# Optimization experiments

Hardware: AMD Instinct MI355X
Metric: run time of the kernel (lower is better)

The kernel has to match this reference:

```python
import jax, jax.numpy as jnp
import numpy as np

NCLASSES = 4
FG_THRESH = 0.5
MEANS = jnp.array([0.0, 0.0, 0.0, 0.0], dtype=jnp.float32)
STDS = jnp.array([0.1, 0.1, 0.2, 0.2], dtype=jnp.float32)
BBOX_INSIDE_W = jnp.array([1.0, 1.0, 1.0, 1.0], dtype=jnp.float32)


def _bbox_overlaps(boxes, gt):
    # boxes: (B,M,4), gt: (B,K,4) -> IoU (B,M,K), faithful to bbox_overlaps_batch
    aw = boxes[..., 2] - boxes[..., 0] + 1.0
    ah = boxes[..., 3] - boxes[..., 1] + 1.0
    gw = gt[..., 2] - gt[..., 0] + 1.0
    gh = gt[..., 3] - gt[..., 1] + 1.0
    area_a = aw * ah                      # (B,M)
    area_g = gw * gh                      # (B,K)
    ix1 = jnp.maximum(boxes[:, :, None, 0], gt[:, None, :, 0])
    iy1 = jnp.maximum(boxes[:, :, None, 1], gt[:, None, :, 1])
    ix2 = jnp.minimum(boxes[:, :, None, 2], gt[:, None, :, 2])
    iy2 = jnp.minimum(boxes[:, :, None, 3], gt[:, None, :, 3])
    iw = jnp.clip(ix2 - ix1 + 1.0, 0.0)
    ih = jnp.clip(iy2 - iy1 + 1.0, 0.0)
    inter = iw * ih                       # (B,M,K)
    ov = inter / (area_a[:, :, None] + area_g[:, None, :] - inter)
    gt_zero = (gw == 1.0) & (gh == 1.0)   # zero-area (padding) gt boxes
    an_zero = (aw == 1.0) & (ah == 1.0)
    ov = jnp.where(gt_zero[:, None, :], 0.0, ov)
    ov = jnp.where(an_zero[:, :, None], -1.0, ov)
    return ov


def _bbox_transform(ex, gt):
    ew = ex[..., 2] - ex[..., 0] + 1.0
    eh = ex[..., 3] - ex[..., 1] + 1.0
    ecx = ex[..., 0] + 0.5 * ew
    ecy = ex[..., 1] + 0.5 * eh
    gw = gt[..., 2] - gt[..., 0] + 1.0
    gh = gt[..., 3] - gt[..., 1] + 1.0
    gcx = gt[..., 0] + 0.5 * gw
    gcy = gt[..., 1] + 0.5 * gh
    dx = (gcx - ecx) / ew
    dy = (gcy - ecy) / eh
    dw = jnp.log(gw / ew)
    dh = jnp.log(gh / eh)
    return jnp.stack([dx, dy, dw, dh], axis=-1)


def setup_inputs() -> dict:
    key = jax.random.key(0)
    B, N, K = 16, 8192, 128
    ks = jax.random.split(key, 9)
    # valid proposal boxes inside an ~1242x375 (KITTI-like) image
    x1 = jax.random.uniform(ks[0], (B, N)) * 1000.0
    y1 = jax.random.uniform(ks[1], (B, N)) * 300.0
    bw = jax.random.uniform(ks[2], (B, N)) * 200.0 + 4.0
    bh = jax.random.uniform(ks[3], (B, N)) * 150.0 + 4.0
    all_rois = jnp.concatenate(
        [jnp.zeros((B, N, 1), jnp.float32),
         jnp.stack([x1, y1, x1 + bw, y1 + bh], axis=-1)], axis=-1)
    gx1 = jax.random.uniform(ks[4], (B, K)) * 1000.0
    gy1 = jax.random.uniform(ks[5], (B, K)) * 300.0
    gw = jax.random.uniform(ks[6], (B, K)) * 200.0 + 8.0
    gh = jax.random.uniform(ks[7], (B, K)) * 150.0 + 8.0
    cls = jax.random.randint(ks[8], (B, K), 1, NCLASSES).astype(jnp.float32)
    gt_boxes = jnp.stack([gx1, gy1, gx1 + gw, gy1 + gh, cls], axis=-1)
    return {"all_rois": all_rois, "gt_boxes": gt_boxes}


def reference(all_rois, gt_boxes):
    B = all_rois.shape[0]
    dt = all_rois.dtype
    # append gt boxes as extra rois: (0, x1, y1, x2, y2)
    gt_append = jnp.concatenate(
        [jnp.zeros_like(gt_boxes[..., :1]), gt_boxes[..., :4]], axis=-1)
    rois = jnp.concatenate([all_rois, gt_append], axis=1)   # (B,M,5)
    M = rois.shape[1]

    ov = _bbox_overlaps(rois[..., 1:5], gt_boxes[..., :4])  # (B,M,K)
    max_ov = ov.max(axis=2)                                 # (B,M)
    gt_assign = jnp.argmax(ov, axis=2)                      # (B,M)
    labels_all = jnp.take_along_axis(gt_boxes[..., 4], gt_assign, axis=1)

    # focal-loss path: fg = ov >= thresh, keep order = [fg asc, bg asc]
    fg = max_ov >= FG_THRESH
    order = jnp.argsort(jnp.where(fg, 0, 1).astype(jnp.int32), axis=1, stable=True)
    fg_count = fg.sum(axis=1)                               # (B,)
    pos = jnp.arange(M)[None, :]

    labels_perm = jnp.take_along_axis(labels_all, order, axis=1)
    labels_batch = jnp.where(pos < fg_count[:, None], labels_perm, 0.0)

    rois_perm = jnp.take_along_axis(rois, order[..., None], axis=1)
    rois_batch = rois_perm.at[..., 0].set(
        jnp.broadcast_to(jnp.arange(B, dtype=dt)[:, None], (B, M)))

    ga_perm = jnp.take_along_axis(gt_assign, order, axis=1)
    gt_rois = jnp.take_along_axis(gt_boxes, ga_perm[..., None], axis=1)  # (B,M,5)

    targets = _bbox_transform(rois_batch[..., 1:5], gt_rois[..., :4])
    targets = (targets - MEANS) / STDS
    bbox_targets = jnp.where((labels_batch > 0)[..., None], targets, 0.0)

    # focal inside weights in ORIGINAL roi order (as in the source), bg zeroed
    focal_w = jnp.where(fg, (1.0 - max_ov) ** 2, 0.0)       # (B,M)
    bbox_inside_weights = jnp.broadcast_to(focal_w[..., None], (B, M, 4))
    bbox_outside_weights = (bbox_inside_weights > 0).astype(dt)

    return (rois_batch, labels_batch, bbox_targets,
            bbox_inside_weights, bbox_outside_weights)
```

## Files before the change

kernel.cpp:

```cpp
#include <hip/hip_runtime.h>
#include <math.h>

#define BB 16
#define NN 8192
#define KK 128
#define MM (NN + KK)
#define NCHUNK 32


__global__ __launch_bounds__(256) void ptl_iou(
    const float* __restrict__ all_rois,
    const float* __restrict__ gt_boxes,
    int* __restrict__ chunk_counts,
    float2* __restrict__ pack,
    float* __restrict__ out_inside,
    float* __restrict__ out_outside)
{
    __shared__ float4 s_box[KK];
    __shared__ int    s_w[4];

    const int b    = blockIdx.y;
    const int cx   = blockIdx.x;
    const int tid  = threadIdx.x;
    const int lane = tid & 63, wv = tid >> 6;

    if (tid < KK) {
        const float* g = gt_boxes + ((size_t)b * KK + tid) * 5;
        float gx1 = g[0], gy1 = g[1], gx2 = g[2], gy2 = g[3];
        float gw = gx2 - gx1 + 1.0f, gh = gy2 - gy1 + 1.0f;
        bool z = (gw == 1.0f) && (gh == 1.0f);
        s_box[tid] = z ? make_float4(1e30f, 1e30f, -1e30f, -1e30f)
                       : make_float4(gx1, gy1, gx2 + 1.0f, gy2 + 1.0f);
    }
    __syncthreads();

    const int i = cx * 256 + tid;
    const float* rp_in = all_rois + ((size_t)b * NN + i) * 5;
    const float x1 = rp_in[1], y1 = rp_in[2], x2 = rp_in[3], y2 = rp_in[4];
    const float X2p = x2 + 1.0f, Y2p = y2 + 1.0f;
    const float aw = X2p - x1, ah = Y2p - y1;
    const float area_a = aw * ah;

    float best = -1e30f;
    int besti = 0;
    #pragma unroll 4
    for (int k = 0; k < KK; ++k) {
        float4 g = s_box[k];
        float area_g = (g.z - g.x) * (g.w - g.y);
        float iw = fmaxf(fminf(X2p, g.z) - fmaxf(x1, g.x), 0.0f);
        float ih = fmaxf(fminf(Y2p, g.w) - fmaxf(y1, g.y), 0.0f);
        float inter = iw * ih;
        float ov = inter / (area_a + area_g - inter);
        if (ov > best) { best = ov; besti = k; }
    }
    if (aw == 1.0f && ah == 1.0f) { best = -1.0f; besti = 0; }

    const bool fg = (best >= 0.5f);

    {
        const size_t idx = (size_t)b * MM + i;
        const float om = 1.0f - best;
        const float w  = fg ? om * om : 0.0f;
        const float ow = (w > 0.0f) ? 1.0f : 0.0f;
        ((float4*)out_inside)[idx]  = make_float4(w, w, w, w);
        ((float4*)out_outside)[idx] = make_float4(ow, ow, ow, ow);
    }
    if (cx == 0 && tid < KK) {
        const size_t idx = (size_t)b * MM + NN + tid;
        ((float4*)out_inside)[idx]  = make_float4(0.f, 0.f, 0.f, 0.f);
        ((float4*)out_outside)[idx] = make_float4(0.f, 0.f, 0.f, 0.f);
    }

    pack[(size_t)b * NN + i] = make_float2(best, __int_as_float(besti));

    unsigned long long m = __ballot(fg ? 1 : 0);
    if (lane == 0) s_w[wv] = __popcll(m);
    __syncthreads();
    if (tid == 0)
        chunk_counts[b * NCHUNK + cx] = s_w[0] + s_w[1] + s_w[2] + s_w[3];
}

__global__ __launch_bounds__(256) void ptl_scatter(
    const float* __restrict__ all_rois,
    const float* __restrict__ gt_boxes,
    const int* __restrict__ chunk_counts,
    const float2* __restrict__ pack,
    float* __restrict__ out_rois,
    float* __restrict__ out_labels,
    float* __restrict__ out_targets)
{
    __shared__ float4 s_box[KK];
    __shared__ float  s_lbl[KK];
    __shared__ int    s_cnt[NCHUNK];
    __shared__ int    s_gtfg[2];
    __shared__ int    s_w[4];

    const int b    = blockIdx.y;
    const int cx   = blockIdx.x;
    const int tid  = threadIdx.x;
    const int lane = tid & 63, wv = tid >> 6;

    bool nondeg = false;
    if (tid < KK) {
        const float* g = gt_boxes + ((size_t)b * KK + tid) * 5;
        float gx1 = g[0], gy1 = g[1], gx2 = g[2], gy2 = g[3];
        float gw = gx2 - gx1 + 1.0f, gh = gy2 - gy1 + 1.0f;
        bool z = (gw == 1.0f) && (gh == 1.0f);
        nondeg = !z;
        s_box[tid] = z ? make_float4(1e30f, 1e30f, -1e30f, -1e30f)
                       : make_float4(gx1, gy1, gx2 + 1.0f, gy2 + 1.0f);
        s_lbl[tid] = g[4];
    }
    {
        unsigned long long nm = __ballot(nondeg);
        if (wv < 2 && lane == 0) s_gtfg[wv] = __popcll(nm);
    }
    if (tid < NCHUNK) s_cnt[tid] = chunk_counts[b * NCHUNK + tid];

    const int i = cx * 256 + tid;
    const float* rp_in = all_rois + ((size_t)b * NN + i) * 5;
    const float x1 = rp_in[1], y1 = rp_in[2], x2 = rp_in[3], y2 = rp_in[4];
    const float2 pk = pack[(size_t)b * NN + i];
    const float best = pk.x;
    const int   besti = __float_as_int(pk.y);
    const bool  fg = (best >= 0.5f);

    unsigned long long m = __ballot(fg ? 1 : 0);
    const int lp = __popcll(m & ((1ull << lane) - 1ull));
    if (lane == 0) s_w[wv] = __popcll(m);
    __syncthreads();

    const int gtFg = s_gtfg[0] + s_gtfg[1];
    int base = 0, pTotal = 0;
    for (int c = 0; c < NCHUNK; ++c) {
        int v = s_cnt[c];
        pTotal += v;
        if (c < cx) base += v;
    }
    const int total = pTotal + gtFg;

    int we = 0;
    for (int w2 = 0; w2 < wv; ++w2) we += s_w[w2];
    const int inChunkExcl = we + lp;

    {
        const int fgBefore = base + inChunkExcl;
        const int p = fg ? fgBefore : (total + i - fgBefore);

        float* rp = out_rois + ((size_t)b * MM + p) * 5;
        rp[0] = (float)b;
        rp[1] = x1; rp[2] = y1; rp[3] = x2; rp[4] = y2;

        float lbl = 0.f;
        float4 t = make_float4(0.f, 0.f, 0.f, 0.f);
        if (fg) {
            lbl = s_lbl[besti];
            if (lbl > 0.0f) {
                float4 g = s_box[besti];
                const float gw = g.z - g.x, gh = g.w - g.y;
                const float gcx = g.x + 0.5f * gw, gcy = g.y + 0.5f * gh;
                const float ew = x2 - x1 + 1.0f, eh = y2 - y1 + 1.0f;
                const float ecx = x1 + 0.5f * ew, ecy = y1 + 0.5f * eh;
                t.x = ((gcx - ecx) / ew) / 0.1f;
                t.y = ((gcy - ecy) / eh) / 0.1f;
                t.z = logf(gw / ew) / 0.2f;
                t.w = logf(gh / eh) / 0.2f;
            }
        }
        out_labels[(size_t)b * MM + p] = lbl;
        ((float4*)out_targets)[(size_t)b * MM + p] = t;
    }

    if (cx == NCHUNK - 1 && tid < KK) {
        const int j = tid;
        const float* g = gt_boxes + ((size_t)b * KK + j) * 5;
        const float gx1 = g[0], gy1 = g[1], gx2 = g[2], gy2 = g[3], cls = g[4];
        const float gw = gx2 - gx1 + 1.0f, gh = gy2 - gy1 + 1.0f;
        const bool nd = !((gw == 1.0f) && (gh == 1.0f));

        unsigned long long m2 = __ballot(nd);
        int pre = __popcll(m2 & ((1ull << lane) - 1ull));
        if (wv == 1) pre += s_gtfg[0];

        const int fgBefore = pTotal + pre;
        const int p = nd ? fgBefore : (total + (NN + j) - fgBefore);

        float* rp = out_rois + ((size_t)b * MM + p) * 5;
        rp[0] = (float)b;
        rp[1] = gx1; rp[2] = gy1; rp[3] = gx2; rp[4] = gy2;
        out_labels[(size_t)b * MM + p] = nd ? cls : 0.0f;
        ((float4*)out_targets)[(size_t)b * MM + p] = make_float4(0.f, 0.f, 0.f, 0.f);
    }
}

extern "C" void kernel_launch(void* const* d_in, const int* in_sizes, int n_in,
                              void* d_out, int out_size, void* d_ws, size_t ws_size,
                              hipStream_t stream) {
    const float* all_rois = (const float*)d_in[0];
    const float* gt_boxes = (const float*)d_in[1];

    float* out = (float*)d_out;
    float* out_rois    = out;
    float* out_labels  = out_rois    + (size_t)BB * MM * 5;
    float* out_targets = out_labels  + (size_t)BB * MM;
    float* out_inside  = out_targets + (size_t)BB * MM * 4;
    float* out_outside = out_inside  + (size_t)BB * MM * 4;

    int*    chunk_counts = (int*)d_ws;
    float2* pack         = (float2*)((char*)d_ws + 8192);

    ptl_iou<<<dim3(NCHUNK, BB), dim3(256, 1, 1), 0, stream>>>(
        all_rois, gt_boxes, chunk_counts, pack, out_inside, out_outside);

    ptl_scatter<<<dim3(NCHUNK, BB), dim3(256, 1, 1), 0, stream>>>(
        all_rois, gt_boxes, chunk_counts, pack,
        out_rois, out_labels, out_targets);
}
```

Measured before the change: 77.47 us.

## Split IoU argmax across four lanes per ROI for more blocks

The IoU kernel now assigns four threads to each ROI, each scanning 32 of the 128 gt boxes, then merges the argmax with xor shuffles using lowest-index tie breaking. The grid grows from 512 to 2048 blocks, and the scatter kernel sums four finer chunk counts to rebuild its per-256 chunk prefix. The aim is more parallelism and better latency hiding in the divide-heavy argmax loop. The cost is that each ROI box is loaded four times and only one lane of each group writes the outputs.

```diff
diff --git a/kernel.cpp b/kernel.cpp
--- a/kernel.cpp
+++ b/kernel.cpp
@@ -6,9 +6,11 @@
 #define KK 128
 #define MM (NN + KK)
 #define NCHUNK 32
-
-
-__global__ __launch_bounds__(256) void ptl_iou(
+#define RPB 64
+#define NCH2 (NN / RPB)
+
+
+__global__ __launch_bounds__(256, 4) void ptl_iou(
     const float* __restrict__ all_rois,
     const float* __restrict__ gt_boxes,
     int* __restrict__ chunk_counts,
@@ -20,9 +22,11 @@
     __shared__ int    s_w[4];
 
     const int b    = blockIdx.y;
-    const int cx   = blockIdx.x;
+    const int c2   = blockIdx.x;
     const int tid  = threadIdx.x;
     const int lane = tid & 63, wv = tid >> 6;
+    const int sub  = tid & 3;
+    const int r    = tid >> 2;
 
     if (tid < KK) {
         const float* g = gt_boxes + ((size_t)b * KK + tid) * 5;
@@ -34,7 +38,7 @@
     }
     __syncthreads();
 
-    const int i = cx * 256 + tid;
+    const int i = c2 * RPB + r;
     const float* rp_in = all_rois + ((size_t)b * NN + i) * 5;
     const float x1 = rp_in[1], y1 = rp_in[2], x2 = rp_in[3], y2 = rp_in[4];
     const float X2p = x2 + 1.0f, Y2p = y2 + 1.0f;
@@ -43,8 +47,10 @@
 
     float best = -1e30f;
     int besti = 0;
+    const int k0 = sub << 5;
     #pragma unroll 4
-    for (int k = 0; k < KK; ++k) {
+    for (int kk = 0; kk < 32; ++kk) {
+        const int k = k0 + kk;
         float4 g = s_box[k];
         float area_g = (g.z - g.x) * (g.w - g.y);
         float iw = fmaxf(fminf(X2p, g.z) - fmaxf(x1, g.x), 0.0f);
@@ -53,31 +59,36 @@
         float ov = inter / (area_a + area_g - inter);
         if (ov > best) { best = ov; besti = k; }
     }
+    #pragma unroll
+    for (int mask = 1; mask <= 2; mask <<= 1) {
+        float ob = __shfl_xor(best, mask);
+        int   oi = __shfl_xor(besti, mask);
+        if (ob > best || (ob == best && oi < besti)) { best = ob; besti = oi; }
+    }
     if (aw == 1.0f && ah == 1.0f) { best = -1.0f; besti = 0; }
 
     const bool fg = (best >= 0.5f);
 
-    {
+    if (sub == 0) {
         const size_t idx = (size_t)b * MM + i;
         const float om = 1.0f - best;
         const float w  = fg ? om * om : 0.0f;
         const float ow = (w > 0.0f) ? 1.0f : 0.0f;
         ((float4*)out_inside)[idx]  = make_float4(w, w, w, w);
         ((float4*)out_outside)[idx] = make_float4(ow, ow, ow, ow);
-    }
-    if (cx == 0 && tid < KK) {
+        pack[(size_t)b * NN + i] = make_float2(best, __int_as_float(besti));
+    }
+    if (c2 == 0 && tid < KK) {
         const size_t idx = (size_t)b * MM + NN + tid;
         ((float4*)out_inside)[idx]  = make_float4(0.f, 0.f, 0.f, 0.f);
         ((float4*)out_outside)[idx] = make_float4(0.f, 0.f, 0.f, 0.f);
     }
 
-    pack[(size_t)b * NN + i] = make_float2(best, __int_as_float(besti));
-
-    unsigned long long m = __ballot(fg ? 1 : 0);
+    unsigned long long m = __ballot((fg && sub == 0) ? 1 : 0);
     if (lane == 0) s_w[wv] = __popcll(m);
     __syncthreads();
     if (tid == 0)
-        chunk_counts[b * NCHUNK + cx] = s_w[0] + s_w[1] + s_w[2] + s_w[3];
+        chunk_counts[b * NCH2 + c2] = s_w[0] + s_w[1] + s_w[2] + s_w[3];
 }
 
 __global__ __launch_bounds__(256) void ptl_scatter(
@@ -115,7 +126,10 @@
         unsigned long long nm = __ballot(nondeg);
         if (wv < 2 && lane == 0) s_gtfg[wv] = __popcll(nm);
     }
-    if (tid < NCHUNK) s_cnt[tid] = chunk_counts[b * NCHUNK + tid];
+    if (tid < NCHUNK) {
+        const int* cc = chunk_counts + b * NCH2 + tid * 4;
+        s_cnt[tid] = cc[0] + cc[1] + cc[2] + cc[3];
+    }
 
     const int i = cx * 256 + tid;
     const float* rp_in = all_rois + ((size_t)b * NN + i) * 5;
@@ -207,9 +221,9 @@
     float* out_outside = out_inside  + (size_t)BB * MM * 4;
 
     int*    chunk_counts = (int*)d_ws;
-    float2* pack         = (float2*)((char*)d_ws + 8192);
-
-    ptl_iou<<<dim3(NCHUNK, BB), dim3(256, 1, 1), 0, stream>>>(
+    float2* pack         = (float2*)((char*)d_ws + 16384);
+
+    ptl_iou<<<dim3(NCH2, BB), dim3(256, 1, 1), 0, stream>>>(
         all_rois, gt_boxes, chunk_counts, pack, out_inside, out_outside);
 
     ptl_scatter<<<dim3(NCHUNK, BB), dim3(256, 1, 1), 0, stream>>>(
```

After: 75.66 us. 1.02x faster.
